# Kernel tuning notes

Measured on AMD Instinct MI355X. Metric: run time of the kernel, lower is better.

The kernel has to match this reference:

```python
import math
import jax, jax.numpy as jnp
from jax import lax
import numpy as np

HIDDEN = 128
KQ_CH = HIDDEN * 3  # 384
H, W = 48, 64
N = 4


def _conv(x, w, pad, dil):
    # NCHW conv, OIHW weights, stride 1
    return lax.conv_general_dilated(
        x, w, window_strides=(1, 1),
        padding=[(pad, pad), (pad, pad)],
        rhs_dilation=(dil, dil),
        dimension_numbers=("NCHW", "OIHW", "NCHW"))


def _lrelu(x):
    return jnp.where(x >= 0, x, 0.2 * x)


def setup_inputs() -> dict:
    key = jax.random.key(0)
    ks = jax.random.split(key, 7)
    s = 0.05
    return {
        "k": jax.random.normal(ks[0], (N, KQ_CH, H, W), jnp.float32),
        "q": jax.random.normal(ks[1], (N, KQ_CH, H, W), jnp.float32),
        "v": jax.random.normal(ks[2], (N, HIDDEN, H, W), jnp.float32),
        "w_value": jax.random.normal(ks[3], (HIDDEN, HIDDEN, 1, 1), jnp.float32) * s,
        "w_out": jax.random.normal(ks[4], (HIDDEN, HIDDEN, 3, 3), jnp.float32) * s,
        "w_ff1": jax.random.normal(ks[5], (HIDDEN, HIDDEN, 3, 3), jnp.float32) * s,
        "w_ff2": jax.random.normal(ks[6], (HIDDEN, HIDDEN, 3, 3), jnp.float32) * s,
    }


def reference(k, q, v, w_value, w_out, w_ff1, w_ff2):
    n, c, h, w = k.shape  # c = kq_channels
    hw = h * w
    # value embedding: 1x1 conv
    val = _conv(v, w_value, 0, 1)  # [n, hidden, h, w]
    kf = k.reshape(n, c, hw)
    qf = q.reshape(n, c, hw)
    # scores[n, key_pos, query_pos] = k^T q / sqrt(c)
    scores = jnp.einsum("nck,ncq->nkq", kf, qf) / math.sqrt(c)
    # softmax over key positions (torch dim=-2)
    p_attn = jax.nn.softmax(scores, axis=1)  # [n, hw, hw]
    # p_val = value @ p_attn
    p_val = jnp.einsum("ndk,nkq->ndq", val.reshape(n, -1, hw), p_attn)
    p_val = p_val.reshape(v.shape)
    # residual update with output_linear (conv3x3 + LeakyReLU)
    v2 = v + _lrelu(_conv(p_val, w_out, 1, 1))
    # dilated-conv feed forward with residual
    ff = _lrelu(_conv(_lrelu(_conv(v2, w_ff1, 2, 2)), w_ff2, 1, 1))
    return v2 + ff
```

## Files before the change

### kernel.cpp

```cpp
#include <hip/hip_runtime.h>

#define NB  4
#define CKQ 384
#define DH  128
#define HH  48
#define WW  64
#define HW  3072

#define NSPLIT 16
#define KSEG  (HW / NSPLIT)
#define BQ 128
#define BK 32
#define VSP 40
#define PTS 40
#define XROW 136

typedef short bf16x8 __attribute__((ext_vector_type(8)));
typedef short b16x4  __attribute__((ext_vector_type(4)));
typedef float f32x4  __attribute__((ext_vector_type(4)));
typedef long  i64;
typedef long  i64x2 __attribute__((ext_vector_type(2)));
typedef unsigned short u16;
typedef unsigned int   u32;
typedef unsigned char  u8;
typedef unsigned long long u64;

__device__ __forceinline__ float b2f(u16 u){
  union { u32 i; float f; } x; x.i = ((u32)u) << 16; return x.f;
}
__device__ __forceinline__ u16 f2b(float f){
  union { float f; u32 i; } x; x.f = f;
  u32 r = (x.i + 0x7fffu + ((x.i >> 16) & 1u)) >> 16;
  return (u16)r;
}
__device__ __forceinline__ u8 f2f8(float f){
  return (u8)(__builtin_amdgcn_cvt_pk_fp8_f32(f, f, 0, false) & 0xff);
}

__global__ __launch_bounds__(256)
void prep(const float* __restrict__ k, const float* __restrict__ q,
          const float* __restrict__ v, const float* __restrict__ wv,
          const float* __restrict__ w0, const float* __restrict__ w1,
          const float* __restrict__ w2,
          u8* __restrict__ kt8, u8* __restrict__ qt8, u8* __restrict__ val8,
          u16* __restrict__ o0, u16* __restrict__ o1, u16* __restrict__ o2){
  __shared__ u8 T[64][392];
  const int b   = blockIdx.x;
  const int tid = threadIdx.x;

  if (b < 384){
    const int yy = b / 48;
    const int bx = b % 48;
    const float* in = (yy < NB) ? k : q;
    u8* outp        = (yy < NB) ? kt8 : qt8;
    const int n  = yy & (NB - 1);
    const int p0 = bx * 64;
    const int tx = tid & 63;
    const int ty = tid >> 6;
    const float* ib = in + (size_t)n * CKQ * HW + p0;
    #pragma unroll 4
    for (int c = ty; c < CKQ; c += 4)
      T[tx][c] = f2f8(ib[(size_t)c * HW + tx]);
    __syncthreads();
    u8* ob = outp + ((size_t)n * HW + p0) * CKQ;
    #pragma unroll
    for (int it = 0; it < 12; ++it){
      int ch  = it * 256 + tid;
      int row = ch / 48;
      int g   = ch - row * 48;
      *(u64*)(ob + (size_t)row * CKQ + g * 8) = *(const u64*)&T[row][g * 8];
    }
  } else if (b < 600){
    const int bb = b - 384;
    const int bx = bb % 72;
    const int wy = bb / 72;
    const float* w = (wy == 0) ? w0 : (wy == 1) ? w1 : w2;
    u16* wt        = (wy == 0) ? o0 : (wy == 1) ? o1 : o2;
    int g    = bx * 256 + tid;
    int fid  = g >> 6;
    int lane = g & 63;
    int l15  = lane & 15, quad = lane >> 4;
    int tap  = fid >> 5;
    int cst  = (fid >> 3) & 3;
    int dt   = fid & 7;
    int d    = dt * 16 + l15;
    u16* dst = wt + (size_t)fid * 512 + lane * 8;
    #pragma unroll
    for (int e = 0; e < 8; ++e){
      int c = cst * 32 + quad * 8 + e;
      dst[e] = f2b(w[((size_t)d * DH + c) * 9 + tap]);
    }
  } else {
    const int bb = b - 600;
    const int px = bb % 12;
    const int db = (bb / 12) & 7;
    const int n  = bb / 96;
    const int p  = px * 256 + tid;
    const int d0 = db * 16;
    const float* vb = v + (size_t)n * DH * HW;
    float acc[16];
    #pragma unroll
    for (int dd = 0; dd < 16; ++dd) acc[dd] = 0.f;
    for (int c = 0; c < DH; ++c){
      float vv = vb[(size_t)c * HW + p];
      #pragma unroll
      for (int dd = 0; dd < 16; ++dd)
        acc[dd] += wv[(d0 + dd) * DH + c] * vv;
    }
    u8* ob = val8 + (size_t)n * DH * HW;
    #pragma unroll
    for (int dd = 0; dd < 16; ++dd)
      ob[(size_t)(d0 + dd) * HW + p] = f2f8(acc[dd]);
  }
}

__global__ __launch_bounds__(256, 3)
void attn8(const u8* __restrict__ kt, const u8* __restrict__ qt,
           const u8* __restrict__ val, u16* __restrict__ outp,
           float* __restrict__ lsum, int seg0){
  __shared__ u8 Ks[BK * CKQ];
  __shared__ u8 Vs[DH * VSP];
  __shared__ u8 Pt[BQ * PTS];

  const int tid  = threadIdx.x;
  const int wv   = tid >> 6;
  const int lane = tid & 63;
  const int quad = lane >> 4;
  const int l15  = lane & 15;
  const int n    = blockIdx.z;
  const int seg  = seg0 + blockIdx.y;
  const int j0   = blockIdx.x * BQ;
  const int jra  = wv * 32 + l15;
  const int jrb  = jra + 16;
  const int ja   = j0 + jra;
  const int jb   = j0 + jrb;

  const u8* qrowa = qt + ((size_t)n * HW + ja) * CKQ;
  const u8* qrowb = qt + ((size_t)n * HW + jb) * CKQ;
  i64 qfa[12], qfb[12];
  #pragma unroll
  for (int cs = 0; cs < 12; ++cs){
    qfa[cs] = *(const i64*)&qrowa[cs * 32 + quad * 8];
    qfb[cs] = *(const i64*)&qrowb[cs * 32 + quad * 8];
  }

  const f32x4 zero = {0.f, 0.f, 0.f, 0.f};
  f32x4 oa[8], obacc[8];
  #pragma unroll
  for (int i = 0; i < 8; ++i){ oa[i] = zero; obacc[i] = zero; }
  float la = 0.f, lbv = 0.f;

  const u8* ktb = kt  + (size_t)n * CKQ * HW;
  const u8* vb  = val + (size_t)n * DH * HW;
  const float scale = 0.05103103630798287f;

  for (int it = 0; it < KSEG / BK; ++it){
    const int i0 = seg * KSEG + it * BK;
    for (int idx = tid; idx < BK * 24; idx += 256){
      int i  = idx / 24;
      int g2 = idx % 24;
      i64x2 dv = *(const i64x2*)&ktb[(size_t)(i0 + i) * CKQ + g2 * 16];
      int g0 = 2 * g2, g1 = g0 + 1;
      int gs0 = (g0 & ~7) | ((g0 ^ i) & 7);
      int gs1 = (g1 & ~7) | ((g1 ^ i) & 7);
      *(i64*)&Ks[i * CKQ + gs0 * 8] = dv[0];
      *(i64*)&Ks[i * CKQ + gs1 * 8] = dv[1];
    }
    for (int idx = tid; idx < DH * 4; idx += 256){
      int dd = idx >> 2;
      int c8 = idx & 3;
      *(i64*)&Vs[dd * VSP + c8 * 8] = *(const i64*)&vb[(size_t)dd * HW + i0 + c8 * 8];
    }
    __syncthreads();

    f32x4 s0a = zero, s1a = zero, s0b = zero, s1b = zero;
    #pragma unroll
    for (int cs = 0; cs < 12; ++cs){
      int g  = 4 * cs + quad;
      int gs = (g & ~7) | ((g ^ l15) & 7);
      i64 a0 = *(const i64*)&Ks[l15 * CKQ + gs * 8];
      i64 a1 = *(const i64*)&Ks[(16 + l15) * CKQ + gs * 8];
      s0a = __builtin_amdgcn_mfma_f32_16x16x32_fp8_fp8(a0, qfa[cs], s0a, 0, 0, 0);
      s1a = __builtin_amdgcn_mfma_f32_16x16x32_fp8_fp8(a1, qfa[cs], s1a, 0, 0, 0);
      s0b = __builtin_amdgcn_mfma_f32_16x16x32_fp8_fp8(a0, qfb[cs], s0b, 0, 0, 0);
      s1b = __builtin_amdgcn_mfma_f32_16x16x32_fp8_fp8(a1, qfb[cs], s1b, 0, 0, 0);
    }

    float pa[8], pb[8]; float tsa = 0.f, tsb = 0.f;
    #pragma unroll
    for (int r = 0; r < 4; ++r){
      pa[r]     = __expf(s0a[r] * scale);
      pa[4 + r] = __expf(s1a[r] * scale);
      pb[r]     = __expf(s0b[r] * scale);
      pb[4 + r] = __expf(s1b[r] * scale);
    }
    #pragma unroll
    for (int i = 0; i < 8; ++i){ tsa += pa[i]; tsb += pb[i]; }
    la += tsa; lbv += tsb;

    u32 wa0 = __builtin_amdgcn_cvt_pk_fp8_f32(pa[0], pa[1], 0, false);
    wa0     = __builtin_amdgcn_cvt_pk_fp8_f32(pa[2], pa[3], wa0, true);
    u32 wa1 = __builtin_amdgcn_cvt_pk_fp8_f32(pa[4], pa[5], 0, false);
    wa1     = __builtin_amdgcn_cvt_pk_fp8_f32(pa[6], pa[7], wa1, true);
    u32 wb0 = __builtin_amdgcn_cvt_pk_fp8_f32(pb[0], pb[1], 0, false);
    wb0     = __builtin_amdgcn_cvt_pk_fp8_f32(pb[2], pb[3], wb0, true);
    u32 wb1 = __builtin_amdgcn_cvt_pk_fp8_f32(pb[4], pb[5], 0, false);
    wb1     = __builtin_amdgcn_cvt_pk_fp8_f32(pb[6], pb[7], wb1, true);
    *(u32*)&Pt[jra * PTS + quad * 4]      = wa0;
    *(u32*)&Pt[jra * PTS + 16 + quad * 4] = wa1;
    *(u32*)&Pt[jrb * PTS + quad * 4]      = wb0;
    *(u32*)&Pt[jrb * PTS + 16 + quad * 4] = wb1;
    __builtin_amdgcn_wave_barrier();

    i64 bpa = *(const i64*)&Pt[jra * PTS + quad * 8];
    i64 bpb = *(const i64*)&Pt[jrb * PTS + quad * 8];
    #pragma unroll
    for (int dt = 0; dt < 8; ++dt){
      i64 av = *(const i64*)&Vs[(dt * 16 + l15) * VSP + quad * 8];
      oa[dt]    = __builtin_amdgcn_mfma_f32_16x16x32_fp8_fp8(av, bpa, oa[dt], 0, 0, 0);
      obacc[dt] = __builtin_amdgcn_mfma_f32_16x16x32_fp8_fp8(av, bpb, obacc[dt], 0, 0, 0);
    }
    __syncthreads();
  }

  la  += __shfl_xor(la, 16);  la  += __shfl_xor(la, 32);
  lbv += __shfl_xor(lbv, 16); lbv += __shfl_xor(lbv, 32);

  u16* obp = outp + ((size_t)(seg * NB + n) * HW) * DH;
  #pragma unroll
  for (int dt = 0; dt < 8; ++dt){
    b16x4 pka = { (short)f2b(oa[dt][0]), (short)f2b(oa[dt][1]),
                  (short)f2b(oa[dt][2]), (short)f2b(oa[dt][3]) };
    b16x4 pkb = { (short)f2b(obacc[dt][0]), (short)f2b(obacc[dt][1]),
                  (short)f2b(obacc[dt][2]), (short)f2b(obacc[dt][3]) };
    *(b16x4*)&obp[(size_t)ja * DH + dt * 16 + quad * 4] = pka;
    *(b16x4*)&obp[(size_t)jb * DH + dt * 16 + quad * 4] = pkb;
  }
  if (quad == 0){
    lsum[(size_t)(seg * NB + n) * HW + ja] = la;
    lsum[(size_t)(seg * NB + n) * HW + jb] = lbv;
  }
}

__global__ __launch_bounds__(256)
void combine(const u16* __restrict__ ob, const float* __restrict__ lb,
             u16* __restrict__ pval_t){
  size_t flat = (size_t)blockIdx.x * 256 + threadIdx.x;
  int d = (int)(flat & 127);
  size_t nj = flat >> 7;
  int j = (int)(nj % HW);
  int n = (int)(nj / HW);
  float acc = 0.f, ls = 0.f;
  #pragma unroll
  for (int s = 0; s < NSPLIT; ++s){
    acc += b2f(ob[((size_t)(s * NB + n) * HW + j) * DH + d]);
    ls  += lb[(size_t)(s * NB + n) * HW + j];
  }
  pval_t[flat] = f2b(acc / ls);
}

template<int DIL, int RESM, int OUTM>
__global__ __launch_bounds__(256, 3)
void mconv(const u16* __restrict__ in_t, const u16* __restrict__ wtf,
           const void* __restrict__ res, void* __restrict__ out){
  __shared__ u16 Xs[3 * 64 * XROW];

  const int tid  = threadIdx.x;
  const int w    = tid >> 6;
  const int lane = tid & 63;
  const int quad = lane >> 4;
  const int l15  = lane & 15;
  const int n    = blockIdx.z;
  const int y    = blockIdx.x;
  const int by   = blockIdx.y;
  const int xw   = w * 16;

  const bf16x8 bz8 = {0,0,0,0,0,0,0,0};
  #pragma unroll
  for (int yi = 0; yi < 3; ++yi){
    int ysrc = y + (yi - 1) * DIL;
    bool ok = (unsigned)ysrc < (unsigned)HH;
    #pragma unroll
    for (int pass = 0; pass < 4; ++pass){
      int ch = pass * 256 + tid;
      int x  = ch >> 4;
      int g  = ch & 15;
      bf16x8 vv = bz8;
      if (ok)
        vv = *(const bf16x8*)&in_t[((size_t)n * HW + ysrc * WW + x) * DH + g * 8];
      *(bf16x8*)&Xs[(yi * 64 + x) * XROW + g * 8] = vv;
    }
  }
  __syncthreads();

  f32x4 acc[2];
  acc[0] = (f32x4){0.f, 0.f, 0.f, 0.f};
  acc[1] = (f32x4){0.f, 0.f, 0.f, 0.f};

  #pragma unroll
  for (int tap = 0; tap < 9; ++tap){
    const int yi = tap / 3;
    const int dx = (tap % 3 - 1) * DIL;
    const int xp = xw + l15 + dx;
    const bool vx = (unsigned)xp < (unsigned)WW;
    const int xc = vx ? xp : 0;
    const u16* xrow = &Xs[(yi * 64 + xc) * XROW];
    #pragma unroll
    for (int cst = 0; cst < 4; ++cst){
      bf16x8 bf = bz8;
      if (vx) bf = *(const bf16x8*)&xrow[cst * 32 + quad * 8];
      #pragma unroll
      for (int dt = 0; dt < 2; ++dt){
        int fid = (tap * 4 + cst) * 8 + by * 2 + dt;
        bf16x8 af = *(const bf16x8*)&wtf[(size_t)fid * 512 + lane * 8];
        acc[dt] = __builtin_amdgcn_mfma_f32_16x16x32_bf16(af, bf, acc[dt], 0, 0, 0);
      }
    }
  }

  const int p = y * WW + xw + l15;
  #pragma unroll
  for (int dt = 0; dt < 2; ++dt){
    const int d0q = by * 32 + dt * 16 + quad * 4;
    float v4[4];
    #pragma unroll
    for (int r = 0; r < 4; ++r){
      float vv = acc[dt][r];
      vv = (vv >= 0.f) ? vv : 0.2f * vv;
      if (RESM == 1)
        vv += ((const float*)res)[((size_t)n * DH + d0q + r) * HW + p];
      v4[r] = vv;
    }
    if (RESM == 2){
      b16x4 rv = *(const b16x4*)&((const u16*)res)[((size_t)n * HW + p) * DH + d0q];
      #pragma unroll
      for (int r = 0; r < 4; ++r) v4[r] += b2f((u16)rv[r]);
    }
    if (OUTM == 0){
      b16x4 pk = { (short)f2b(v4[0]), (short)f2b(v4[1]),
                   (short)f2b(v4[2]), (short)f2b(v4[3]) };
      *(b16x4*)&((u16*)out)[((size_t)n * HW + p) * DH + d0q] = pk;
    } else {
      #pragma unroll
      for (int r = 0; r < 4; ++r)
        ((float*)out)[((size_t)n * DH + d0q + r) * HW + p] = v4[r];
    }
  }
}

extern "C" void kernel_launch(void* const* d_in, const int* in_sizes, int n_in,
                              void* d_out, int out_size, void* d_ws, size_t ws_size,
                              hipStream_t stream){
  const float* k    = (const float*)d_in[0];
  const float* q    = (const float*)d_in[1];
  const float* v    = (const float*)d_in[2];
  const float* wv   = (const float*)d_in[3];
  const float* wout = (const float*)d_in[4];
  const float* wff1 = (const float*)d_in[5];
  const float* wff2 = (const float*)d_in[6];
  float* out = (float*)d_out;

  const size_t TEN  = (size_t)NB * DH * HW;
  const size_t KTEN = (size_t)NB * CKQ * HW;
  const size_t WT   = (size_t)9 * DH * DH;
  u8*  kt8    = (u8*)d_ws;
  u8*  qt8    = kt8 + KTEN;
  u8*  val8   = qt8 + KTEN;
  u16* wt1    = (u16*)(val8 + TEN);
  u16* wt2    = wt1 + WT;
  u16* wt3    = wt2 + WT;
  u16* pval_t = wt3 + WT;
  u16* v2_t   = pval_t + TEN;
  u16* tmid_t = v2_t + TEN;
  u16* ob     = tmid_t + TEN;
  float* lb   = (float*)(ob + (size_t)NSPLIT * TEN);

  prep   <<<dim3(984), 256, 0, stream>>>(k, q, v, wv, wout, wff1, wff2,
                                         kt8, qt8, val8, wt1, wt2, wt3);
  attn8  <<<dim3(HW / BQ, NSPLIT / 2, NB), 256, 0, stream>>>(kt8, qt8, val8, ob, lb, 0);
  attn8  <<<dim3(HW / BQ, NSPLIT / 2, NB), 256, 0, stream>>>(kt8, qt8, val8, ob, lb, NSPLIT / 2);
  combine<<<dim3((unsigned)(TEN / 256)), 256, 0, stream>>>(ob, lb, pval_t);
  mconv<1, 1, 0><<<dim3(48, 4, NB), 256, 0, stream>>>(pval_t, wt1, (const void*)v,    (void*)v2_t);
  mconv<2, 0, 0><<<dim3(48, 4, NB), 256, 0, stream>>>(v2_t,   wt2, (const void*)nullptr, (void*)tmid_t);
  mconv<1, 2, 1><<<dim3(48, 4, NB), 256, 0, stream>>>(tmid_t, wt3, (const void*)v2_t, (void*)out);
}
```

Before: 232.0 us.

## Double-buffer K/V tiles in attention via register prefetch, merge split launches

```diff
diff --git a/kernel.cpp b/kernel.cpp
--- a/kernel.cpp
+++ b/kernel.cpp
@@ -11,6 +11,7 @@
 #define KSEG  (HW / NSPLIT)
 #define BQ 128
 #define BK 32
+#define NIT (KSEG / BK)
 #define VSP 40
 #define PTS 40
 #define XROW 136
@@ -58,7 +59,7 @@
     const int tx = tid & 63;
     const int ty = tid >> 6;
     const float* ib = in + (size_t)n * CKQ * HW + p0;
-    #pragma unroll 4
+    #pragma unroll 8
     for (int c = ty; c < CKQ; c += 4)
       T[tx][c] = f2f8(ib[(size_t)c * HW + tx]);
     __syncthreads();
@@ -101,6 +102,7 @@
     float acc[16];
     #pragma unroll
     for (int dd = 0; dd < 16; ++dd) acc[dd] = 0.f;
+    #pragma unroll 8
     for (int c = 0; c < DH; ++c){
       float vv = vb[(size_t)c * HW + p];
       #pragma unroll
@@ -117,9 +119,9 @@
 __global__ __launch_bounds__(256, 3)
 void attn8(const u8* __restrict__ kt, const u8* __restrict__ qt,
            const u8* __restrict__ val, u16* __restrict__ outp,
-           float* __restrict__ lsum, int seg0){
-  __shared__ u8 Ks[BK * CKQ];
-  __shared__ u8 Vs[DH * VSP];
+           float* __restrict__ lsum){
+  __shared__ u8 Ks[2][BK * CKQ];
+  __shared__ u8 Vs[2][DH * VSP];
   __shared__ u8 Pt[BQ * PTS];
 
   const int tid  = threadIdx.x;
@@ -128,13 +130,19 @@
   const int quad = lane >> 4;
   const int l15  = lane & 15;
   const int n    = blockIdx.z;
-  const int seg  = seg0 + blockIdx.y;
+  const int seg  = blockIdx.y;
   const int j0   = blockIdx.x * BQ;
   const int jra  = wv * 32 + l15;
   const int jrb  = jra + 16;
   const int ja   = j0 + jra;
   const int jb   = j0 + jrb;
 
+  const u8* ktb = kt  + (size_t)n * CKQ * HW;
+  const u8* vb  = val + (size_t)n * DH * HW;
+
+  const int ki0 = tid, ki1 = tid + 256, ki2 = tid + 512;
+  const int vi0 = tid, vi1 = tid + 256;
+
   const u8* qrowa = qt + ((size_t)n * HW + ja) * CKQ;
   const u8* qrowb = qt + ((size_t)n * HW + jb) * CKQ;
   i64 qfa[12], qfb[12];
@@ -150,36 +158,52 @@
   for (int i = 0; i < 8; ++i){ oa[i] = zero; obacc[i] = zero; }
   float la = 0.f, lbv = 0.f;
 
-  const u8* ktb = kt  + (size_t)n * CKQ * HW;
-  const u8* vb  = val + (size_t)n * DH * HW;
   const float scale = 0.05103103630798287f;
 
-  for (int it = 0; it < KSEG / BK; ++it){
-    const int i0 = seg * KSEG + it * BK;
-    for (int idx = tid; idx < BK * 24; idx += 256){
-      int i  = idx / 24;
-      int g2 = idx % 24;
-      i64x2 dv = *(const i64x2*)&ktb[(size_t)(i0 + i) * CKQ + g2 * 16];
-      int g0 = 2 * g2, g1 = g0 + 1;
-      int gs0 = (g0 & ~7) | ((g0 ^ i) & 7);
-      int gs1 = (g1 & ~7) | ((g1 ^ i) & 7);
-      *(i64*)&Ks[i * CKQ + gs0 * 8] = dv[0];
-      *(i64*)&Ks[i * CKQ + gs1 * 8] = dv[1];
-    }
-    for (int idx = tid; idx < DH * 4; idx += 256){
-      int dd = idx >> 2;
-      int c8 = idx & 3;
-      *(i64*)&Vs[dd * VSP + c8 * 8] = *(const i64*)&vb[(size_t)dd * HW + i0 + c8 * 8];
-    }
-    __syncthreads();
+  i64x2 kr0, kr1, kr2; i64 vr0, vr1;
+  {
+    const int i0 = seg * KSEG;
+    kr0 = *(const i64x2*)&ktb[(size_t)(i0 + ki0 / 24) * CKQ + (ki0 % 24) * 16];
+    kr1 = *(const i64x2*)&ktb[(size_t)(i0 + ki1 / 24) * CKQ + (ki1 % 24) * 16];
+    kr2 = *(const i64x2*)&ktb[(size_t)(i0 + ki2 / 24) * CKQ + (ki2 % 24) * 16];
+    vr0 = *(const i64*)&vb[(size_t)(vi0 >> 2) * HW + i0 + (vi0 & 3) * 8];
+    vr1 = *(const i64*)&vb[(size_t)(vi1 >> 2) * HW + i0 + (vi1 & 3) * 8];
+  }
+  #pragma unroll
+  for (int r = 0; r < 3; ++r){
+    int idx = tid + r * 256;
+    int i = idx / 24, g2 = idx % 24;
+    int g0 = 2 * g2, g1 = g0 + 1;
+    int gs0 = (g0 & ~7) | ((g0 ^ i) & 7);
+    int gs1 = (g1 & ~7) | ((g1 ^ i) & 7);
+    i64x2 dv = (r == 0) ? kr0 : (r == 1) ? kr1 : kr2;
+    *(i64*)&Ks[0][i * CKQ + gs0 * 8] = dv[0];
+    *(i64*)&Ks[0][i * CKQ + gs1 * 8] = dv[1];
+  }
+  *(i64*)&Vs[0][(vi0 >> 2) * VSP + (vi0 & 3) * 8] = vr0;
+  *(i64*)&Vs[0][(vi1 >> 2) * VSP + (vi1 & 3) * 8] = vr1;
+  __syncthreads();
+
+  for (int it = 0; it < NIT; ++it){
+    const int cur = it & 1, nxt = cur ^ 1;
+    const bool more = (it + 1 < NIT);
+
+    if (more){
+      const int i0n = seg * KSEG + (it + 1) * BK;
+      kr0 = *(const i64x2*)&ktb[(size_t)(i0n + ki0 / 24) * CKQ + (ki0 % 24) * 16];
+      kr1 = *(const i64x2*)&ktb[(size_t)(i0n + ki1 / 24) * CKQ + (ki1 % 24) * 16];
+      kr2 = *(const i64x2*)&ktb[(size_t)(i0n + ki2 / 24) * CKQ + (ki2 % 24) * 16];
+      vr0 = *(const i64*)&vb[(size_t)(vi0 >> 2) * HW + i0n + (vi0 & 3) * 8];
+      vr1 = *(const i64*)&vb[(size_t)(vi1 >> 2) * HW + i0n + (vi1 & 3) * 8];
+    }
 
     f32x4 s0a = zero, s1a = zero, s0b = zero, s1b = zero;
     #pragma unroll
     for (int cs = 0; cs < 12; ++cs){
       int g  = 4 * cs + quad;
       int gs = (g & ~7) | ((g ^ l15) & 7);
-      i64 a0 = *(const i64*)&Ks[l15 * CKQ + gs * 8];
-      i64 a1 = *(const i64*)&Ks[(16 + l15) * CKQ + gs * 8];
+      i64 a0 = *(const i64*)&Ks[cur][l15 * CKQ + gs * 8];
+      i64 a1 = *(const i64*)&Ks[cur][(16 + l15) * CKQ + gs * 8];
       s0a = __builtin_amdgcn_mfma_f32_16x16x32_fp8_fp8(a0, qfa[cs], s0a, 0, 0, 0);
       s1a = __builtin_amdgcn_mfma_f32_16x16x32_fp8_fp8(a1, qfa[cs], s1a, 0, 0, 0);
       s0b = __builtin_amdgcn_mfma_f32_16x16x32_fp8_fp8(a0, qfb[cs], s0b, 0, 0, 0);
@@ -216,9 +240,25 @@
     i64 bpb = *(const i64*)&Pt[jrb * PTS + quad * 8];
     #pragma unroll
     for (int dt = 0; dt < 8; ++dt){
-      i64 av = *(const i64*)&Vs[(dt * 16 + l15) * VSP + quad * 8];
+      i64 av = *(const i64*)&Vs[cur][(dt * 16 + l15) * VSP + quad * 8];
       oa[dt]    = __builtin_amdgcn_mfma_f32_16x16x32_fp8_fp8(av, bpa, oa[dt], 0, 0, 0);
       obacc[dt] = __builtin_amdgcn_mfma_f32_16x16x32_fp8_fp8(av, bpb, obacc[dt], 0, 0, 0);
+    }
+
+    if (more){
+      #pragma unroll
+      for (int r = 0; r < 3; ++r){
+        int idx = tid + r * 256;
+        int i = idx / 24, g2 = idx % 24;
+        int g0 = 2 * g2, g1 = g0 + 1;
+        int gs0 = (g0 & ~7) | ((g0 ^ i) & 7);
+        int gs1 = (g1 & ~7) | ((g1 ^ i) & 7);
+        i64x2 dv = (r == 0) ? kr0 : (r == 1) ? kr1 : kr2;
+        *(i64*)&Ks[nxt][i * CKQ + gs0 * 8] = dv[0];
+        *(i64*)&Ks[nxt][i * CKQ + gs1 * 8] = dv[1];
+      }
+      *(i64*)&Vs[nxt][(vi0 >> 2) * VSP + (vi0 & 3) * 8] = vr0;
+      *(i64*)&Vs[nxt][(vi1 >> 2) * VSP + (vi1 & 3) * 8] = vr1;
     }
     __syncthreads();
   }
@@ -377,8 +417,7 @@
 
   prep   <<<dim3(984), 256, 0, stream>>>(k, q, v, wv, wout, wff1, wff2,
                                          kt8, qt8, val8, wt1, wt2, wt3);
-  attn8  <<<dim3(HW / BQ, NSPLIT / 2, NB), 256, 0, stream>>>(kt8, qt8, val8, ob, lb, 0);
-  attn8  <<<dim3(HW / BQ, NSPLIT / 2, NB), 256, 0, stream>>>(kt8, qt8, val8, ob, lb, NSPLIT / 2);
+  attn8  <<<dim3(HW / BQ, NSPLIT, NB), 256, 0, stream>>>(kt8, qt8, val8, ob, lb);
   combine<<<dim3((unsigned)(TEN / 256)), 256, 0, stream>>>(ob, lb, pval_t);
   mconv<1, 1, 0><<<dim3(48, 4, NB), 256, 0, stream>>>(pval_t, wt1, (const void*)v,    (void*)v2_t);
   mconv<2, 0, 0><<<dim3(48, 4, NB), 256, 0, stream>>>(v2_t,   wt2, (const void*)nullptr, (void*)tmid_t);
```

After: 255.0 us. 1.1x slower.
